# Performance work log

Hardware: AMD Instinct MI355X
Metric: run time of the kernel (lower is better)

Reference implementation:

```python
import jax, jax.numpy as jnp
import numpy as np

N_SRC = 2_000_000
N_TAR = 2_000_000

def _make_covs(key, n):
    # 3x3 SPD block embedded in a 4x4 (last row/col zero), as in GICP covariances
    A = jax.random.normal(key, (n, 3, 3), dtype=jnp.float32)
    cov3 = 0.1 * jnp.einsum('nij,nkj->nik', A, A) + 0.1 * jnp.eye(3, dtype=jnp.float32)
    covs = jnp.zeros((n, 4, 4), dtype=jnp.float32)
    return covs.at[:, :3, :3].set(cov3)

def setup_inputs() -> dict:
    key = jax.random.key(0)
    k1, k2, k3, k4, k5, k6 = jax.random.split(key, 6)
    # homogeneous points (x, y, z, 1)
    src_xyz = jax.random.normal(k1, (N_SRC, 3), dtype=jnp.float32) * 5.0
    tar_xyz = jax.random.normal(k2, (N_TAR, 3), dtype=jnp.float32) * 5.0
    ones_s = jnp.ones((N_SRC, 1), dtype=jnp.float32)
    ones_t = jnp.ones((N_TAR, 1), dtype=jnp.float32)
    src_points = jnp.concatenate([src_xyz, ones_s], axis=1)
    tar_points = jnp.concatenate([tar_xyz, ones_t], axis=1)
    covs_src = _make_covs(k3, N_SRC)
    covs_tar = _make_covs(k4, N_TAR)
    # transformation: near-identity SE(3)-ish 4x4 (param in the original model)
    transformation = jnp.eye(4, dtype=jnp.float32) + 0.01 * jax.random.normal(k5, (4, 4), dtype=jnp.float32)
    # nearest-neighbor indices (kdtree result in the original, non-differentiable)
    nearest_indices = jax.random.randint(k6, (N_SRC,), 0, N_TAR, dtype=jnp.int64 if jax.config.jax_enable_x64 else jnp.int32)
    return {
        'transformation': transformation,
        'src_points': src_points,
        'tar_points': tar_points,
        'covs_src': covs_src,
        'covs_tar': covs_tar,
        'nearest_indices': nearest_indices,
    }

def reference(transformation, src_points, tar_points, covs_src, covs_tar, nearest_indices):
    # transformed_src_points = src_points @ T  (N,4)
    transformed_src = src_points @ transformation
    # gather KNN-matched target points / covariances
    sel_tar = tar_points[nearest_indices]          # (N,4)
    sel_covs_tar = covs_tar[nearest_indices]       # (N,4,4)
    # T @ C_src @ T^T per point
    tcov = jnp.einsum('ij,njk,lk->nil', transformation, covs_src, transformation)
    RCR = sel_covs_tar + tcov                      # (N,4,4)
    inv_RCR = jnp.linalg.inv(RCR[:, :3, :3])       # (N,3,3)
    res = sel_tar[:, :3] - transformed_src[:, :3]  # (N,3)
    maha = jnp.einsum('ni,nij,nj->n', res, inv_RCR, res)
    return 0.5 * jnp.mean(maha)
```

## Files before the change

### kernel.cpp

```cpp
#include <hip/hip_runtime.h>

#define GRID_BLOCKS 1024
#define BLOCK       256

__device__ __forceinline__ float gicp_point(
    int i,
    const float t00, const float t01, const float t02,
    const float t10, const float t11, const float t12,
    const float t20, const float t21, const float t22,
    const float t30, const float t31, const float t32,
    const float4* __restrict__ src, const float4* __restrict__ tar,
    const float4* __restrict__ cs,  const float4* __restrict__ ct,
    const int*    __restrict__ idx)
{
    const float4 s  = src[i];
    const int    j  = idx[i];
    const float4 tp = tar[j];

    const float ts0 = s.x * t00 + s.y * t10 + s.z * t20 + s.w * t30;
    const float ts1 = s.x * t01 + s.y * t11 + s.z * t21 + s.w * t31;
    const float ts2 = s.x * t02 + s.y * t12 + s.z * t22 + s.w * t32;
    const float r0 = tp.x - ts0;
    const float r1 = tp.y - ts1;
    const float r2 = tp.z - ts2;

    const size_t bi = (size_t)i * 4;
    const float4 c0 = cs[bi + 0];
    const float4 c1 = cs[bi + 1];
    const float4 c2 = cs[bi + 2];

    const float u00 = t00*c0.x + t01*c1.x + t02*c2.x;
    const float u01 = t00*c0.y + t01*c1.y + t02*c2.y;
    const float u02 = t00*c0.z + t01*c1.z + t02*c2.z;
    const float u10 = t10*c0.x + t11*c1.x + t12*c2.x;
    const float u11 = t10*c0.y + t11*c1.y + t12*c2.y;
    const float u12 = t10*c0.z + t11*c1.z + t12*c2.z;
    const float u20 = t20*c0.x + t21*c1.x + t22*c2.x;
    const float u21 = t20*c0.y + t21*c1.y + t22*c2.y;
    const float u22 = t20*c0.z + t21*c1.z + t22*c2.z;

    const float tc00 = u00*t00 + u01*t01 + u02*t02;
    const float tc01 = u00*t10 + u01*t11 + u02*t12;
    const float tc02 = u00*t20 + u01*t21 + u02*t22;
    const float tc11 = u10*t10 + u11*t11 + u12*t12;
    const float tc12 = u10*t20 + u11*t21 + u12*t22;
    const float tc22 = u20*t20 + u21*t21 + u22*t22;

    const size_t bj = (size_t)j * 4;
    const float4 d0 = ct[bj + 0];
    const float4 d1 = ct[bj + 1];
    const float4 d2 = ct[bj + 2];

    const float a = d0.x + tc00;
    const float b = d0.y + tc01;
    const float c = d0.z + tc02;
    const float d = d1.y + tc11;
    const float e = d1.z + tc12;
    const float f = d2.z + tc22;

    const float A00 = d * f - e * e;
    const float A01 = c * e - b * f;
    const float A02 = b * e - c * d;
    const float A11 = a * f - c * c;
    const float A12 = b * c - a * e;
    const float A22 = a * d - b * b;

    const float det = a * A00 + b * A01 + c * A02;

    const float num = r0 * r0 * A00 + r1 * r1 * A11 + r2 * r2 * A22
                    + 2.0f * (r0 * r1 * A01 + r0 * r2 * A02 + r1 * r2 * A12);

    return num / det;
}

__global__ __launch_bounds__(BLOCK) void gicp_maha_kernel(
    const float*  __restrict__ T,
    const float4* __restrict__ src,
    const float4* __restrict__ tar,
    const float4* __restrict__ cs,
    const float4* __restrict__ ct,
    const int*    __restrict__ idx,
    float*        __restrict__ partial,
    int n)
{
    const float t00 = T[0],  t01 = T[1],  t02 = T[2];
    const float t10 = T[4],  t11 = T[5],  t12 = T[6];
    const float t20 = T[8],  t21 = T[9],  t22 = T[10];
    const float t30 = T[12], t31 = T[13], t32 = T[14];

    const int stride = GRID_BLOCKS * BLOCK;
    int i = blockIdx.x * BLOCK + threadIdx.x;

    float local = 0.0f;
    for (; i + 3 * stride < n; i += 4 * stride) {
        float v0 = gicp_point(i,            t00,t01,t02,t10,t11,t12,t20,t21,t22,t30,t31,t32, src,tar,cs,ct,idx);
        float v1 = gicp_point(i +   stride, t00,t01,t02,t10,t11,t12,t20,t21,t22,t30,t31,t32, src,tar,cs,ct,idx);
        float v2 = gicp_point(i + 2*stride, t00,t01,t02,t10,t11,t12,t20,t21,t22,t30,t31,t32, src,tar,cs,ct,idx);
        float v3 = gicp_point(i + 3*stride, t00,t01,t02,t10,t11,t12,t20,t21,t22,t30,t31,t32, src,tar,cs,ct,idx);
        local += (v0 + v1) + (v2 + v3);
    }
    for (; i < n; i += stride)
        local += gicp_point(i, t00,t01,t02,t10,t11,t12,t20,t21,t22,t30,t31,t32, src,tar,cs,ct,idx);

    for (int off = 32; off > 0; off >>= 1)
        local += __shfl_down(local, off, 64);

    __shared__ float wsum[BLOCK / 64];
    const int wave = threadIdx.x >> 6;
    if ((threadIdx.x & 63) == 0) wsum[wave] = local;
    __syncthreads();
    if (threadIdx.x == 0) {
        float s = wsum[0];
        #pragma unroll
        for (int w = 1; w < BLOCK / 64; ++w) s += wsum[w];
        partial[blockIdx.x] = s;
    }
}

__global__ __launch_bounds__(256) void gicp_finalize_kernel(
    const float* __restrict__ partial, float* __restrict__ out, double scale)
{
    double s = 0.0;
    for (int k = threadIdx.x; k < GRID_BLOCKS; k += 256)
        s += (double)partial[k];
    for (int off = 32; off > 0; off >>= 1)
        s += __shfl_down(s, off, 64);
    __shared__ double wsum[4];
    const int wave = threadIdx.x >> 6;
    if ((threadIdx.x & 63) == 0) wsum[wave] = s;
    __syncthreads();
    if (threadIdx.x == 0)
        out[0] = (float)((wsum[0] + wsum[1] + wsum[2] + wsum[3]) * scale);
}

extern "C" void kernel_launch(void* const* d_in, const int* in_sizes, int n_in,
                              void* d_out, int out_size, void* d_ws, size_t ws_size,
                              hipStream_t stream) {
    const float*  T   = (const float*)d_in[0];
    const float4* src = (const float4*)d_in[1];
    const float4* tar = (const float4*)d_in[2];
    const float4* cs  = (const float4*)d_in[3];
    const float4* ct  = (const float4*)d_in[4];
    const int*    idx = (const int*)d_in[5];
    const int n = in_sizes[1] / 4;

    float* partial = (float*)d_ws;

    gicp_maha_kernel<<<GRID_BLOCKS, BLOCK, 0, stream>>>(T, src, tar, cs, ct,
                                                        idx, partial, n);
    gicp_finalize_kernel<<<1, 256, 0, stream>>>(partial, (float*)d_out,
                                                0.5 / (double)n);
}
```

Baseline: 339.3 us.

## Batch all loads up front with nontemporal streaming and one-chunk-per-block grid

Replaces the persistent grid-stride loop with a grid sized to cover n, where each thread handles four points. All loads are issued before any compute: the index and the streaming source and covariance data use nontemporal loads, followed by the gathered target loads. The aim is more memory-level parallelism, and keeping streamed data from evicting the randomly gathered target data from cache. It launches about 2000 blocks instead of 1024, so the partial-sum buffer and the finalize kernel grow with the block count, and higher register pressure could reduce occupancy.

```diff
diff --git a/kernel.cpp b/kernel.cpp
--- a/kernel.cpp
+++ b/kernel.cpp
@@ -1,86 +1,19 @@
 #include <hip/hip_runtime.h>
 
-#define GRID_BLOCKS 1024
-#define BLOCK       256
+#define BLOCK  256
+#define UNROLL 4
+#define CHUNK  (BLOCK * UNROLL)
 
-__device__ __forceinline__ float gicp_point(
-    int i,
-    const float t00, const float t01, const float t02,
-    const float t10, const float t11, const float t12,
-    const float t20, const float t21, const float t22,
-    const float t30, const float t31, const float t32,
-    const float4* __restrict__ src, const float4* __restrict__ tar,
-    const float4* __restrict__ cs,  const float4* __restrict__ ct,
-    const int*    __restrict__ idx)
-{
-    const float4 s  = src[i];
-    const int    j  = idx[i];
-    const float4 tp = tar[j];
+typedef float f4 __attribute__((ext_vector_type(4)));
 
-    const float ts0 = s.x * t00 + s.y * t10 + s.z * t20 + s.w * t30;
-    const float ts1 = s.x * t01 + s.y * t11 + s.z * t21 + s.w * t31;
-    const float ts2 = s.x * t02 + s.y * t12 + s.z * t22 + s.w * t32;
-    const float r0 = tp.x - ts0;
-    const float r1 = tp.y - ts1;
-    const float r2 = tp.z - ts2;
-
-    const size_t bi = (size_t)i * 4;
-    const float4 c0 = cs[bi + 0];
-    const float4 c1 = cs[bi + 1];
-    const float4 c2 = cs[bi + 2];
-
-    const float u00 = t00*c0.x + t01*c1.x + t02*c2.x;
-    const float u01 = t00*c0.y + t01*c1.y + t02*c2.y;
-    const float u02 = t00*c0.z + t01*c1.z + t02*c2.z;
-    const float u10 = t10*c0.x + t11*c1.x + t12*c2.x;
-    const float u11 = t10*c0.y + t11*c1.y + t12*c2.y;
-    const float u12 = t10*c0.z + t11*c1.z + t12*c2.z;
-    const float u20 = t20*c0.x + t21*c1.x + t22*c2.x;
-    const float u21 = t20*c0.y + t21*c1.y + t22*c2.y;
-    const float u22 = t20*c0.z + t21*c1.z + t22*c2.z;
-
-    const float tc00 = u00*t00 + u01*t01 + u02*t02;
-    const float tc01 = u00*t10 + u01*t11 + u02*t12;
-    const float tc02 = u00*t20 + u01*t21 + u02*t22;
-    const float tc11 = u10*t10 + u11*t11 + u12*t12;
-    const float tc12 = u10*t20 + u11*t21 + u12*t22;
-    const float tc22 = u20*t20 + u21*t21 + u22*t22;
-
-    const size_t bj = (size_t)j * 4;
-    const float4 d0 = ct[bj + 0];
-    const float4 d1 = ct[bj + 1];
-    const float4 d2 = ct[bj + 2];
-
-    const float a = d0.x + tc00;
-    const float b = d0.y + tc01;
-    const float c = d0.z + tc02;
-    const float d = d1.y + tc11;
-    const float e = d1.z + tc12;
-    const float f = d2.z + tc22;
-
-    const float A00 = d * f - e * e;
-    const float A01 = c * e - b * f;
-    const float A02 = b * e - c * d;
-    const float A11 = a * f - c * c;
-    const float A12 = b * c - a * e;
-    const float A22 = a * d - b * b;
-
-    const float det = a * A00 + b * A01 + c * A02;
-
-    const float num = r0 * r0 * A00 + r1 * r1 * A11 + r2 * r2 * A22
-                    + 2.0f * (r0 * r1 * A01 + r0 * r2 * A02 + r1 * r2 * A12);
-
-    return num / det;
-}
-
-__global__ __launch_bounds__(BLOCK) void gicp_maha_kernel(
-    const float*  __restrict__ T,
-    const float4* __restrict__ src,
-    const float4* __restrict__ tar,
-    const float4* __restrict__ cs,
-    const float4* __restrict__ ct,
-    const int*    __restrict__ idx,
-    float*        __restrict__ partial,
+__global__ __launch_bounds__(BLOCK, 4) void gicp_maha_kernel(
+    const float* __restrict__ T,
+    const f4*    __restrict__ src,
+    const f4*    __restrict__ tar,
+    const f4*    __restrict__ cs,
+    const f4*    __restrict__ ct,
+    const int*   __restrict__ idx,
+    float*       __restrict__ partial,
     int n)
 {
     const float t00 = T[0],  t01 = T[1],  t02 = T[2];
@@ -88,19 +21,99 @@
     const float t20 = T[8],  t21 = T[9],  t22 = T[10];
     const float t30 = T[12], t31 = T[13], t32 = T[14];
 
-    const int stride = GRID_BLOCKS * BLOCK;
-    int i = blockIdx.x * BLOCK + threadIdx.x;
+    const int base = blockIdx.x * CHUNK + threadIdx.x;
+
+    bool valid[UNROLL];
+    int  ii[UNROLL];
+    int  jj[UNROLL];
+    f4   sv[UNROLL];
+    f4   c0v[UNROLL], c1v[UNROLL], c2v[UNROLL];
+    f4   tpv[UNROLL];
+    f4   d0v[UNROLL], d1v[UNROLL], d2v[UNROLL];
+
+    #pragma unroll
+    for (int k = 0; k < UNROLL; ++k) {
+        int i = base + k * BLOCK;
+        valid[k] = (i < n);
+        ii[k] = valid[k] ? i : 0;
+        jj[k] = __builtin_nontemporal_load(idx + ii[k]);
+    }
+    #pragma unroll
+    for (int k = 0; k < UNROLL; ++k)
+        sv[k] = __builtin_nontemporal_load(src + ii[k]);
+    #pragma unroll
+    for (int k = 0; k < UNROLL; ++k) {
+        const size_t bi = (size_t)ii[k] * 4;
+        c0v[k] = __builtin_nontemporal_load(cs + bi + 0);
+        c1v[k] = __builtin_nontemporal_load(cs + bi + 1);
+        c2v[k] = __builtin_nontemporal_load(cs + bi + 2);
+    }
+
+    #pragma unroll
+    for (int k = 0; k < UNROLL; ++k) {
+        const int j = jj[k];
+        const size_t bj = (size_t)j * 4;
+        tpv[k] = tar[j];
+        d0v[k] = ct[bj + 0];
+        d1v[k] = ct[bj + 1];
+        d2v[k] = ct[bj + 2];
+    }
 
     float local = 0.0f;
-    for (; i + 3 * stride < n; i += 4 * stride) {
-        float v0 = gicp_point(i,            t00,t01,t02,t10,t11,t12,t20,t21,t22,t30,t31,t32, src,tar,cs,ct,idx);
-        float v1 = gicp_point(i +   stride, t00,t01,t02,t10,t11,t12,t20,t21,t22,t30,t31,t32, src,tar,cs,ct,idx);
-        float v2 = gicp_point(i + 2*stride, t00,t01,t02,t10,t11,t12,t20,t21,t22,t30,t31,t32, src,tar,cs,ct,idx);
-        float v3 = gicp_point(i + 3*stride, t00,t01,t02,t10,t11,t12,t20,t21,t22,t30,t31,t32, src,tar,cs,ct,idx);
-        local += (v0 + v1) + (v2 + v3);
+    #pragma unroll
+    for (int k = 0; k < UNROLL; ++k) {
+        const f4 s  = sv[k];
+        const f4 tp = tpv[k];
+
+        const float ts0 = s.x * t00 + s.y * t10 + s.z * t20 + s.w * t30;
+        const float ts1 = s.x * t01 + s.y * t11 + s.z * t21 + s.w * t31;
+        const float ts2 = s.x * t02 + s.y * t12 + s.z * t22 + s.w * t32;
+        const float r0 = tp.x - ts0;
+        const float r1 = tp.y - ts1;
+        const float r2 = tp.z - ts2;
+
+        const f4 c0 = c0v[k], c1 = c1v[k], c2 = c2v[k];
+
+        const float u00 = t00*c0.x + t01*c1.x + t02*c2.x;
+        const float u01 = t00*c0.y + t01*c1.y + t02*c2.y;
+        const float u02 = t00*c0.z + t01*c1.z + t02*c2.z;
+        const float u10 = t10*c0.x + t11*c1.x + t12*c2.x;
+        const float u11 = t10*c0.y + t11*c1.y + t12*c2.y;
+        const float u12 = t10*c0.z + t11*c1.z + t12*c2.z;
+        const float u20 = t20*c0.x + t21*c1.x + t22*c2.x;
+        const float u21 = t20*c0.y + t21*c1.y + t22*c2.y;
+        const float u22 = t20*c0.z + t21*c1.z + t22*c2.z;
+
+        const float tc00 = u00*t00 + u01*t01 + u02*t02;
+        const float tc01 = u00*t10 + u01*t11 + u02*t12;
+        const float tc02 = u00*t20 + u01*t21 + u02*t22;
+        const float tc11 = u10*t10 + u11*t11 + u12*t12;
+        const float tc12 = u10*t20 + u11*t21 + u12*t22;
+        const float tc22 = u20*t20 + u21*t21 + u22*t22;
+
+        const f4 d0 = d0v[k], d1 = d1v[k], d2 = d2v[k];
+
+        const float a = d0.x + tc00;
+        const float b = d0.y + tc01;
+        const float c = d0.z + tc02;
+        const float d = d1.y + tc11;
+        const float e = d1.z + tc12;
+        const float f = d2.z + tc22;
+
+        const float A00 = d * f - e * e;
+        const float A01 = c * e - b * f;
+        const float A02 = b * e - c * d;
+        const float A11 = a * f - c * c;
+        const float A12 = b * c - a * e;
+        const float A22 = a * d - b * b;
+
+        const float det = a * A00 + b * A01 + c * A02;
+
+        const float num = r0 * r0 * A00 + r1 * r1 * A11 + r2 * r2 * A22
+                        + 2.0f * (r0 * r1 * A01 + r0 * r2 * A02 + r1 * r2 * A12);
+
+        local += valid[k] ? (num / det) : 0.0f;
     }
-    for (; i < n; i += stride)
-        local += gicp_point(i, t00,t01,t02,t10,t11,t12,t20,t21,t22,t30,t31,t32, src,tar,cs,ct,idx);
 
     for (int off = 32; off > 0; off >>= 1)
         local += __shfl_down(local, off, 64);
@@ -118,10 +131,11 @@
 }
 
 __global__ __launch_bounds__(256) void gicp_finalize_kernel(
-    const float* __restrict__ partial, float* __restrict__ out, double scale)
+    const float* __restrict__ partial, float* __restrict__ out,
+    int nblocks, double scale)
 {
     double s = 0.0;
-    for (int k = threadIdx.x; k < GRID_BLOCKS; k += 256)
+    for (int k = threadIdx.x; k < nblocks; k += 256)
         s += (double)partial[k];
     for (int off = 32; off > 0; off >>= 1)
         s += __shfl_down(s, off, 64);
@@ -136,18 +150,19 @@
 extern "C" void kernel_launch(void* const* d_in, const int* in_sizes, int n_in,
                               void* d_out, int out_size, void* d_ws, size_t ws_size,
                               hipStream_t stream) {
-    const float*  T   = (const float*)d_in[0];
-    const float4* src = (const float4*)d_in[1];
-    const float4* tar = (const float4*)d_in[2];
-    const float4* cs  = (const float4*)d_in[3];
-    const float4* ct  = (const float4*)d_in[4];
-    const int*    idx = (const int*)d_in[5];
+    const float* T   = (const float*)d_in[0];
+    const f4*    src = (const f4*)d_in[1];
+    const f4*    tar = (const f4*)d_in[2];
+    const f4*    cs  = (const f4*)d_in[3];
+    const f4*    ct  = (const f4*)d_in[4];
+    const int*   idx = (const int*)d_in[5];
     const int n = in_sizes[1] / 4;
 
+    const int grid = (n + CHUNK - 1) / CHUNK;
     float* partial = (float*)d_ws;
 
-    gicp_maha_kernel<<<GRID_BLOCKS, BLOCK, 0, stream>>>(T, src, tar, cs, ct,
-                                                        idx, partial, n);
+    gicp_maha_kernel<<<grid, BLOCK, 0, stream>>>(T, src, tar, cs, ct, idx,
+                                                 partial, n);
     gicp_finalize_kernel<<<1, 256, 0, stream>>>(partial, (float*)d_out,
-                                                0.5 / (double)n);
+                                                grid, 0.5 / (double)n);
 }
```

New measurement: 351.2 us. +3.5%, slower.
